# Kernel tuning notes

Hardware: AMD Instinct MI355X
Metric: run time of the kernel (lower is better)

## Reference

```python
import jax, jax.numpy as jnp
import numpy as np
import math

NUM_HEADS = 16
NUM_BUCKETS = 32
MAX_DISTANCE = 128
ALPHA = 32.0


def _rel_bucket(rel_pos):
    # bidirectional T5-style bucketing
    nb = NUM_BUCKETS // 2
    buckets = (rel_pos > 0).astype(jnp.int32) * nb
    rel_pos = jnp.abs(rel_pos)
    max_exact = nb // 2
    is_small = rel_pos < max_exact
    large = max_exact + (
        jnp.log(rel_pos.astype(jnp.float32) / max_exact + 1e-06)
        / math.log(MAX_DISTANCE / max_exact)
        * (nb - max_exact)
    ).astype(jnp.int32)
    large = jnp.minimum(large, nb - 1)
    return buckets + jnp.where(is_small, rel_pos, large)


def setup_inputs() -> dict:
    key = jax.random.key(0)
    ks = jax.random.split(key, 12)
    T, B, E = 1024, 4, 1024
    hd = E // NUM_HEADS
    s = 0.02
    f32 = jnp.float32
    return {
        "query": jax.random.normal(ks[0], (T, B, E), f32),
        "q_w": jax.random.normal(ks[1], (E, E), f32) * s,
        "q_b": jnp.zeros((E,), f32),
        "k_w": jax.random.normal(ks[2], (E, E), f32) * s,
        "k_b": jnp.zeros((E,), f32),
        "v_w": jax.random.normal(ks[3], (E, E), f32) * s,
        "v_b": jnp.zeros((E,), f32),
        "out_w": jax.random.normal(ks[4], (E, E), f32) * s,
        "out_b": jnp.zeros((E,), f32),
        "rel_emb": jax.random.normal(ks[5], (NUM_BUCKETS, NUM_HEADS), f32) * 0.1,
        "grep_w": jax.random.normal(ks[6], (hd, 8), f32) * s,
        "grep_b": jnp.zeros((8,), f32),
        "grep_a": jnp.ones((1, NUM_HEADS, 1, 1), f32),
        "bias_k": jax.random.normal(ks[7], (1, 1, E), f32) * s,
        "bias_v": jax.random.normal(ks[8], (1, 1, E), f32) * s,
    }


def reference(query, q_w, q_b, k_w, k_b, v_w, v_b, out_w, out_b,
              rel_emb, grep_w, grep_b, grep_a, bias_k, bias_v):
    tgt_len, bsz, embed_dim = query.shape
    nh = NUM_HEADS
    hd = embed_dim // nh
    scaling = hd ** (-0.5)

    # projections (self-attention: q, k, v all from query)
    q = query @ q_w + q_b
    k = query @ k_w + k_b
    v = query @ v_w + v_b
    q = q * scaling / ALPHA

    # bias_kv concat along sequence axis
    k = jnp.concatenate([k, jnp.tile(bias_k, (1, bsz, 1))], axis=0)
    v = jnp.concatenate([v, jnp.tile(bias_v, (1, bsz, 1))], axis=0)

    # faithful to source layout (including its (bsz,tgt,nh,hd)->(bsz*nh,tgt,hd) reshape)
    q = jnp.transpose(q.reshape(tgt_len, bsz, nh, hd), (1, 0, 2, 3)).reshape(bsz * nh, tgt_len, hd)
    k = jnp.transpose(k.reshape(-1, bsz, nh, hd), (1, 0, 2, 3)).reshape(bsz * nh, -1, hd)
    v = jnp.transpose(v.reshape(-1, bsz, nh, hd), (1, 0, 2, 3)).reshape(bsz * nh, -1, hd)
    src_len = k.shape[1]

    # [B*H, T, S]
    attn_weights = jnp.einsum("bth,bsh->bts", q, k)

    # T5-style relative position bias
    rel_pos = jnp.arange(src_len)[None, :] - jnp.arange(tgt_len)[:, None]
    buckets = _rel_bucket(rel_pos)                        # [T, S]
    pb = rel_emb[buckets]                                 # [T, S, H]
    pb = jnp.transpose(pb, (2, 0, 1))                     # [H, T, S]
    pb = jnp.tile(pb[None], (bsz, 1, 1, 1)).reshape(bsz * nh, tgt_len, src_len)

    # GRU-style gating of the position bias
    query_layer = q.reshape(bsz, nh, tgt_len, hd) * ALPHA / scaling
    gate = jax.nn.sigmoid((query_layer @ grep_w + grep_b).sum(-1, keepdims=True))
    gate = (gate * grep_a).reshape(bsz * nh, tgt_len, 1)
    attn_weights = attn_weights + gate * pb

    probs = jax.nn.softmax(attn_weights, axis=-1)
    attn = jnp.einsum("bts,bsh->bth", probs, v)           # [B*H, T, hd]
    attn = attn.reshape(bsz, nh, tgt_len, hd)
    attn = jnp.transpose(attn, (2, 0, 1, 3)).reshape(tgt_len, bsz, embed_dim)
    return attn @ out_w + out_b
```

## Files before the change

### kernel.cpp

```cpp
#include <hip/hip_runtime.h>
#include <stdint.h>

typedef unsigned short u16;
typedef __attribute__((ext_vector_type(4))) float  f32x4;
typedef __attribute__((ext_vector_type(8))) short  short8;
typedef __attribute__((ext_vector_type(8))) u16    u16x8;
typedef __attribute__((ext_vector_type(4))) u16    u16x4;
typedef __attribute__((ext_vector_type(4))) float  fv4;

#define T_LEN 1024
#define EMB   1024
#define SPAD  1088
#define LOG2E 1.44269504f

#define OFF_QX   (0ull)
#define OFF_VT   (0ull)
#define OFF_WT   (8912896ull)
#define OFF_QB   (17301504ull)
#define OFF_KB   (25690112ull)
#define OFF_VB   (34603008ull)
#define OFF_AT   (34603008ull)
#define OFF_GATE (43515904ull)
#define OFF_PB   (43778048ull)
#define OFF_AUX  (43909120ull)

__device__ __forceinline__ u16 f2bf(float f) {
  uint32_t u = __builtin_bit_cast(uint32_t, f);
  u += 0x7FFFu + ((u >> 16) & 1u);
  return (u16)(u >> 16);
}
__device__ __forceinline__ float bf2f(u16 s) {
  uint32_t u = ((uint32_t)s) << 16;
  return __builtin_bit_cast(float, u);
}
__device__ __forceinline__ void gld_lds16(const void* gp, void* lp) {
  __builtin_amdgcn_global_load_lds(
      (const __attribute__((address_space(1))) uint32_t*)(uintptr_t)(gp),
      (__attribute__((address_space(3))) uint32_t*)(uintptr_t)(lp),
      16, 0, 0);
}

__global__ void k_convert_q(const float* __restrict__ q, u16* __restrict__ qx) {
  int i = blockIdx.x * 256 + threadIdx.x;
  fv4 v = *((const fv4*)q + i);
  u16x4 o = { f2bf(v[0]), f2bf(v[1]), f2bf(v[2]), f2bf(v[3]) };
  *((u16x4*)qx + i) = o;
}

__global__ void k_transw(const float* __restrict__ w0, const float* __restrict__ w1,
                         const float* __restrict__ w2, const float* __restrict__ w3,
                         u16* __restrict__ wt) {
  __shared__ float tile[32][33];
  const int z = blockIdx.z;
  const float* w = (z == 0) ? w0 : (z == 1) ? w1 : (z == 2) ? w2 : w3;
  const int r0 = blockIdx.y * 32, c0 = blockIdx.x * 32;
  const int tx = threadIdx.x, ty = threadIdx.y;
  #pragma unroll
  for (int j = 0; j < 32; j += 8)
    tile[ty + j][tx] = w[(size_t)(r0 + ty + j) * EMB + c0 + tx];
  __syncthreads();
  u16* o = wt + (size_t)z * EMB * EMB;
  #pragma unroll
  for (int j = 0; j < 32; j += 8)
    o[(size_t)(c0 + ty + j) * EMB + r0 + tx] = f2bf(tile[tx][ty + j]);
}

__global__ void k_pb(const float* __restrict__ rel_emb, float* __restrict__ pbtab,
                     const float* __restrict__ grep_w, const float* __restrict__ grep_b,
                     float* __restrict__ aux) {
  int i = blockIdx.x * 256 + threadIdx.x;
  int rel = 1024 - i;
  int bucket = (rel > 0) ? 16 : 0;
  int r = rel < 0 ? -rel : rel;
  int bidx;
  if (r < 8) bidx = r;
  else {
    float lf = __logf((float)r / 8.0f + 1e-6f) * (1.0f / logf(16.0f)) * 8.0f;
    int large = 8 + (int)lf;
    bidx = large < 15 ? large : 15;
  }
  bucket += bidx;
  #pragma unroll
  for (int h = 0; h < 16; ++h) pbtab[h * 2048 + i] = rel_emb[bucket * 16 + h] * LOG2E;
  if (blockIdx.x == 0) {
    if (threadIdx.x < 64) {
      float s = 0.f;
      #pragma unroll
      for (int j = 0; j < 8; ++j) s += grep_w[threadIdx.x * 8 + j];
      aux[threadIdx.x] = s;
    } else if (threadIdx.x == 64) {
      float s = 0.f;
      #pragma unroll
      for (int j = 0; j < 8; ++j) s += grep_b[j];
      aux[64] = s;
    }
  }
}

__device__ __forceinline__ void gemm_tile(const u16* __restrict__ A, const u16* __restrict__ Bt,
                                          int m0, int n0, u16* As, u16* Bs, f32x4 acc[4][4]) {
  const int tid = threadIdx.x;
  const int lane = tid & 63, wid = tid >> 6;
  const int wm = wid >> 1, wn = wid & 1;
  const int l15 = lane & 15, l4 = lane >> 4;
  for (int kt = 0; kt < EMB; kt += 32) {
    #pragma unroll
    for (int i = 0; i < 2; ++i) {
      int cw = wid * 64 + i * 256;
      int c = cw + lane;
      int row = c >> 2, cb = c & 3;
      gld_lds16(A  + (size_t)(m0 + row) * EMB + kt + cb * 8, (char*)As + (size_t)cw * 16);
      gld_lds16(Bt + (size_t)(n0 + row) * EMB + kt + cb * 8, (char*)Bs + (size_t)cw * 16);
    }
    __syncthreads();
    short8 a[4], b[4];
    #pragma unroll
    for (int f = 0; f < 4; ++f) {
      a[f] = *(const short8*)(As + (wm * 64 + f * 16 + l15) * 32 + l4 * 8);
      b[f] = *(const short8*)(Bs + (wn * 64 + f * 16 + l15) * 32 + l4 * 8);
    }
    #pragma unroll
    for (int mi = 0; mi < 4; ++mi)
      #pragma unroll
      for (int ni = 0; ni < 4; ++ni)
        acc[mi][ni] = __builtin_amdgcn_mfma_f32_16x16x32_bf16(a[mi], b[ni], acc[mi][ni], 0, 0, 0);
    __syncthreads();
  }
}

__global__ __launch_bounds__(256, 2) void k_qkv_gemm(const u16* __restrict__ qx, const u16* __restrict__ wt,
    const float* __restrict__ qbias, const float* __restrict__ kbias, const float* __restrict__ vbias,
    u16* __restrict__ qb, u16* __restrict__ kb, u16* __restrict__ vb) {
  __shared__ u16 lds[8192];
  f32x4 acc[4][4];
  #pragma unroll
  for (int i = 0; i < 4; ++i)
    #pragma unroll
    for (int j = 0; j < 4; ++j) acc[i][j] = (f32x4){0.f, 0.f, 0.f, 0.f};
  const int m0 = blockIdx.y * 128, n0g = blockIdx.x * 128;
  gemm_tile(qx, wt, m0, n0g, lds, lds + 4096, acc);
  const int z = n0g >> 10;
  const float* bias = (z == 0) ? qbias : (z == 1) ? kbias : vbias;
  const int lane = threadIdx.x & 63, wid = threadIdx.x >> 6;
  const int wm = wid >> 1, wn = wid & 1, l15 = lane & 15, l4 = lane >> 4;
  #pragma unroll
  for (int ni = 0; ni < 4; ++ni) {
    int colg = n0g + wn * 64 + ni * 16 + l15;
    int col = colg & 1023;
    float bv = bias[col];
    int h = col >> 6, d = col & 63;
    #pragma unroll
    for (int mi = 0; mi < 4; ++mi) {
      #pragma unroll
      for (int r = 0; r < 4; ++r) {
        int row = m0 + wm * 64 + mi * 16 + l4 * 4 + r;
        int t = row >> 2, b = row & 3;
        float v = acc[mi][ni][r] + bv;
        if (z == 0) {
          int x = b * 16 + (t >> 6), u = ((t & 63) << 4) + h;
          qb[((size_t)x * 1024 + u) * 64 + d] = f2bf(v * (LOG2E / 256.0f));
        } else {
          int w = t * 16 + h;
          int j = w / 1025;
          int u = w - j * 1025;
          int x = b * 16 + j;
          if (z == 1) kb[((size_t)x * SPAD + u) * 64 + d] = f2bf(v);
          else        vb[((size_t)x * SPAD + u) * 64 + d] = f2bf(v);
        }
      }
    }
  }
}

__global__ void k_biaskv(const float* __restrict__ bias_k, const float* __restrict__ bias_v,
                         u16* __restrict__ kb, u16* __restrict__ vb) {
  int i = blockIdx.x * 256 + threadIdx.x;
  int b = i >> 10, h = (i >> 6) & 15, d = i & 63;
  int x = b * 16 + 15, u = 1009 + h;
  kb[((size_t)x * SPAD + u) * 64 + d] = f2bf(bias_k[h * 64 + d]);
  vb[((size_t)x * SPAD + u) * 64 + d] = f2bf(bias_v[h * 64 + d]);
}

__global__ void k_vtrans(const u16* __restrict__ vb, u16* __restrict__ vt) {
  __shared__ u16 t[64][72];
  const int x = blockIdx.y;
  const int u0 = blockIdx.x * 64;
  const int tid = threadIdx.x;
  const int ur = tid >> 2, c0 = (tid & 3) * 16;
  const u16* src = vb + ((size_t)x * SPAD + u0 + ur) * 64 + c0;
  u16x8 a0 = *(const u16x8*)(src);
  u16x8 a1 = *(const u16x8*)(src + 8);
  *(u16x8*)(&t[ur][c0]) = a0;
  *(u16x8*)(&t[ur][c0 + 8]) = a1;
  __syncthreads();
  const int d = tid >> 2, j = tid & 3;
  u16x8 o0, o1;
  #pragma unroll
  for (int i = 0; i < 8; ++i) o0[i] = t[j * 16 + i][d];
  #pragma unroll
  for (int i = 0; i < 8; ++i) o1[i] = t[j * 16 + 8 + i][d];
  u16* dst = vt + ((size_t)x * 64 + d) * SPAD + u0 + j * 16;
  *(u16x8*)(dst) = o0;
  *(u16x8*)(dst + 8) = o1;
}

__global__ void k_gate(const u16* __restrict__ qb, const float* __restrict__ aux,
                       const float* __restrict__ grep_a, float* __restrict__ gate) {
  int tid = threadIdx.x, lane = tid & 63, wid = tid >> 6;
  int row0 = (blockIdx.x * 4 + wid) * 8;
  int sub = lane >> 3, d0 = (lane & 7) * 8;
  int item = row0 + sub;
  u16x8 q8 = *(const u16x8*)(qb + (size_t)item * 64 + d0);
  float acc = 0.f;
  #pragma unroll
  for (int j = 0; j < 8; ++j) acc += bf2f(q8[j]) * aux[d0 + j];
  acc += __shfl_xor(acc, 1);
  acc += __shfl_xor(acc, 2);
  acc += __shfl_xor(acc, 4);
  if ((lane & 7) == 0) {
    float v = acc * (256.0f / LOG2E) + aux[64];
    float s = 1.0f / (1.0f + __expf(-v));
    gate[item] = s * grep_a[(item >> 10) & 15];
  }
}

__global__ __launch_bounds__(256, 2) void k_attn(const u16* __restrict__ qb, const u16* __restrict__ kb,
    const u16* __restrict__ vt, const float* __restrict__ gate, const float* __restrict__ pbt,
    u16* __restrict__ at) {
  __shared__ float pb_s[2048];
  __shared__ u16 Ksh[2 * 4096];
  __shared__ u16 Vsh[2 * 4096];
  __shared__ u16 Psh[4 * 2048];
  const int tid = threadIdx.x, lane = tid & 63, wid = tid >> 6;
  const int l15 = lane & 15, l4 = lane >> 4;
  const int bid = blockIdx.x;
  const int x = (bid & 7) + ((bid >> 6) << 3);
  const int tblk = (bid >> 3) & 7;
  const int h = x & 15, b = x >> 4;
  const int qrow0 = tblk * 128 + wid * 32;

  #pragma unroll
  for (int i = 0; i < 2; ++i) {
    int idx = (tid + i * 256) * 4;
    *(fv4*)(pb_s + idx) = *(const fv4*)(pbt + (size_t)h * 2048 + idx);
  }

  short8 qa[2][2];
  #pragma unroll
  for (int pf = 0; pf < 2; ++pf)
    #pragma unroll
    for (int ks = 0; ks < 2; ++ks)
      qa[pf][ks] = *(const short8*)(qb + ((size_t)x * 1024 + qrow0 + pf * 16 + l15) * 64 + ks * 32 + l4 * 8);
  float g[2][4];
  #pragma unroll
  for (int pf = 0; pf < 2; ++pf)
    #pragma unroll
    for (int r = 0; r < 4; ++r)
      g[pf][r] = gate[(size_t)x * 1024 + qrow0 + pf * 16 + l4 * 4 + r];

  const u16* kbx = kb + (size_t)x * SPAD * 64;
  const u16* vtx = vt + (size_t)x * 64 * SPAD;
  const int ra = tid >> 3, sa = tid & 7;
  const int rb = ra + 32;
  const u16* sK0 = kbx + ra * 64 + ((sa * 8) ^ ((ra & 7) << 3));
  const u16* sK1 = kbx + rb * 64 + ((sa * 8) ^ ((rb & 7) << 3));
  const u16* sV0 = vtx + (size_t)ra * SPAD + ((sa * 8) ^ ((ra & 7) << 3));
  const u16* sV1 = vtx + (size_t)rb * SPAD + ((sa * 8) ^ ((rb & 7) << 3));

  const int swz = (l15 & 7) << 3;
  int kfO[4][2];
  #pragma unroll
  for (int f = 0; f < 4; ++f)
    #pragma unroll
    for (int ks = 0; ks < 2; ++ks)
      kfO[f][ks] = (f * 16 + l15) * 64 + ((ks * 32 + l4 * 8) ^ swz);
  int paO[2][2];
  #pragma unroll
  for (int pf = 0; pf < 2; ++pf)
    #pragma unroll
    for (int ks = 0; ks < 2; ++ks)
      paO[pf][ks] = (pf * 16 + l15) * 64 + ((ks * 32 + l4 * 8) ^ swz);
  u16* Pw = Psh + wid * 2048;

  f32x4 O[2][4];
  float l_[2][4];
  #pragma unroll
  for (int pf = 0; pf < 2; ++pf) {
    #pragma unroll
    for (int df = 0; df < 4; ++df) O[pf][df] = (f32x4){0.f, 0.f, 0.f, 0.f};
    #pragma unroll
    for (int r = 0; r < 4; ++r) l_[pf][r] = 0.f;
  }

  gld_lds16(sK0, (char*)Ksh + wid * 1024);
  gld_lds16(sK1, (char*)Ksh + 4096 + wid * 1024);
  gld_lds16(sV0, (char*)Vsh + wid * 1024);
  gld_lds16(sV1, (char*)Vsh + 4096 + wid * 1024);
  sK0 += 4096; sK1 += 4096; sV0 += 64; sV1 += 64;
  __asm__ volatile("s_waitcnt vmcnt(0)" ::: "memory");
  __syncthreads();

  int cur = 0;
  for (int ic = 0; ic < 16; ++ic) {
    const int nxt = cur ^ 1;
    char* Kn = (char*)(Ksh + nxt * 4096);
    char* Vn = (char*)(Vsh + nxt * 4096);
    if (ic < 15) {
      gld_lds16(sK0, Kn + wid * 1024);
      gld_lds16(sK1, Kn + 4096 + wid * 1024);
      gld_lds16(sV0, Vn + wid * 1024);
      gld_lds16(sV1, Vn + 4096 + wid * 1024);
      sK0 += 4096; sK1 += 4096; sV0 += 64; sV1 += 64;
    } else if (wid < 2) {
      int ro = (wid * 64 + lane) >> 3, so = lane & 7;
      gld_lds16(kbx + (size_t)(1024 + ro) * 64 + so * 8, Kn + wid * 1024);
    }
    const u16* Kc = Ksh + cur * 4096;
    const u16* Vc = Vsh + cur * 4096;

    f32x4 sc[2][4];
    #pragma unroll
    for (int pf = 0; pf < 2; ++pf)
      #pragma unroll
      for (int nf = 0; nf < 4; ++nf) sc[pf][nf] = (f32x4){0.f, 0.f, 0.f, 0.f};
    #pragma unroll
    for (int nf = 0; nf < 4; ++nf)
      #pragma unroll
      for (int ks = 0; ks < 2; ++ks) {
        short8 kf = *(const short8*)(Kc + kfO[nf][ks]);
        sc[0][nf] = __builtin_amdgcn_mfma_f32_16x16x32_bf16(qa[0][ks], kf, sc[0][nf], 0, 0, 0);
        sc[1][nf] = __builtin_amdgcn_mfma_f32_16x16x32_bf16(qa[1][ks], kf, sc[1][nf], 0, 0, 0);
      }

    #pragma unroll
    for (int pf = 0; pf < 2; ++pf)
      #pragma unroll
      for (int nf = 0; nf < 4; ++nf) {
        const int base = 1024 + qrow0 + pf * 16 + l4 * 4 - (ic * 64 + nf * 16 + l15);
        #pragma unroll
        for (int r = 0; r < 4; ++r) {
          float sv = sc[pf][nf][r] + g[pf][r] * pb_s[base + r];
          float p = exp2f(sv);
          l_[pf][r] += p;
          const int prow = pf * 16 + l4 * 4 + r;
          Pw[prow * 64 + ((nf * 16 + l15) ^ ((prow & 7) << 3))] =
              (u16)(__builtin_bit_cast(uint32_t, p) >> 16);
        }
      }
    __asm__ volatile("s_waitcnt lgkmcnt(0)" ::: "memory");
    __builtin_amdgcn_sched_barrier(0);

    #pragma unroll
    for (int ks = 0; ks < 2; ++ks) {
      short8 pa0 = *(const short8*)(Pw + paO[0][ks]);
      short8 pa1 = *(const short8*)(Pw + paO[1][ks]);
      #pragma unroll
      for (int df = 0; df < 4; ++df) {
        short8 vbf = *(const short8*)(Vc + kfO[df][ks]);
        O[0][df] = __builtin_amdgcn_mfma_f32_16x16x32_bf16(pa0, vbf, O[0][df], 0, 0, 0);
        O[1][df] = __builtin_amdgcn_mfma_f32_16x16x32_bf16(pa1, vbf, O[1][df], 0, 0, 0);
      }
    }
    __asm__ volatile("s_waitcnt vmcnt(0)" ::: "memory");
    __syncthreads();
    cur = nxt;
  }

  const u16* Kt = Ksh + cur * 4096;
  short8 kt0 = *(const short8*)(Kt + l15 * 64 + l4 * 8);
  short8 kt1 = *(const short8*)(Kt + l15 * 64 + 32 + l4 * 8);
  f32x4 sc0[2];
  #pragma unroll
  for (int pf = 0; pf < 2; ++pf) {
    sc0[pf] = (f32x4){0.f, 0.f, 0.f, 0.f};
    sc0[pf] = __builtin_amdgcn_mfma_f32_16x16x32_bf16(qa[pf][0], kt0, sc0[pf], 0, 0, 0);
    sc0[pf] = __builtin_amdgcn_mfma_f32_16x16x32_bf16(qa[pf][1], kt1, sc0[pf], 0, 0, 0);
  }
  float vtail[4];
  #pragma unroll
  for (int df = 0; df < 4; ++df)
    vtail[df] = bf2f(vt[((size_t)x * 64 + df * 16 + l15) * SPAD + 1024]);

  float pt[2][4], linv[2][4];
  #pragma unroll
  for (int pf = 0; pf < 2; ++pf)
    #pragma unroll
    for (int r = 0; r < 4; ++r) {
      float dotv = __shfl(sc0[pf][r], lane & 48);
      int t = qrow0 + pf * 16 + l4 * 4 + r;
      float se = dotv + g[pf][r] * pb_s[t];
      float p = exp2f(se);
      float ls = l_[pf][r];
      ls += __shfl_xor(ls, 1);
      ls += __shfl_xor(ls, 2);
      ls += __shfl_xor(ls, 4);
      ls += __shfl_xor(ls, 8);
      pt[pf][r] = p;
      linv[pf][r] = 1.0f / (ls + p);
    }

  #pragma unroll
  for (int pf = 0; pf < 2; ++pf)
    #pragma unroll
    for (int df = 0; df < 4; ++df)
      #pragma unroll
      for (int r = 0; r < 4; ++r) {
        int t = qrow0 + pf * 16 + l4 * 4 + r;
        float o = (O[pf][df][r] + pt[pf][r] * vtail[df]) * linv[pf][r];
        at[((size_t)(t * 4 + b)) * 1024 + h * 64 + df * 16 + l15] = f2bf(o);
      }
}

__global__ __launch_bounds__(256, 2) void k_out_gemm(const u16* __restrict__ at, const u16* __restrict__ wt3,
                                                     const float* __restrict__ obias, float* __restrict__ out) {
  __shared__ u16 lds[8192];
  f32x4 acc[4][4];
  #pragma unroll
  for (int i = 0; i < 4; ++i)
    #pragma unroll
    for (int j = 0; j < 4; ++j) acc[i][j] = (f32x4){0.f, 0.f, 0.f, 0.f};
  const int m0 = blockIdx.y * 128, n0 = blockIdx.x * 128;
  gemm_tile(at, wt3, m0, n0, lds, lds + 4096, acc);
  const int lane = threadIdx.x & 63, wid = threadIdx.x >> 6;
  const int wm = wid >> 1, wn = wid & 1, l15 = lane & 15, l4 = lane >> 4;
  #pragma unroll
  for (int ni = 0; ni < 4; ++ni) {
    int col = n0 + wn * 64 + ni * 16 + l15;
    float bv = obias[col];
    #pragma unroll
    for (int mi = 0; mi < 4; ++mi) {
      #pragma unroll
      for (int r = 0; r < 4; ++r) {
        int row = m0 + wm * 64 + mi * 16 + l4 * 4 + r;
        out[(size_t)row * 1024 + col] = acc[mi][ni][r] + bv;
      }
    }
  }
}

extern "C" void kernel_launch(void* const* d_in, const int* in_sizes, int n_in,
                              void* d_out, int out_size, void* d_ws, size_t ws_size,
                              hipStream_t stream) {
  const float* query   = (const float*)d_in[0];
  const float* q_w     = (const float*)d_in[1];
  const float* q_b     = (const float*)d_in[2];
  const float* k_w     = (const float*)d_in[3];
  const float* k_b     = (const float*)d_in[4];
  const float* v_w     = (const float*)d_in[5];
  const float* v_b     = (const float*)d_in[6];
  const float* out_w   = (const float*)d_in[7];
  const float* out_b   = (const float*)d_in[8];
  const float* rel_emb = (const float*)d_in[9];
  const float* grep_w  = (const float*)d_in[10];
  const float* grep_b  = (const float*)d_in[11];
  const float* grep_a  = (const float*)d_in[12];
  const float* bias_k  = (const float*)d_in[13];
  const float* bias_v  = (const float*)d_in[14];
  char* ws = (char*)d_ws;
  u16*   qx  = (u16*)(ws + OFF_QX);
  u16*   vt  = (u16*)(ws + OFF_VT);
  u16*   wt  = (u16*)(ws + OFF_WT);
  u16*   qb  = (u16*)(ws + OFF_QB);
  u16*   kb  = (u16*)(ws + OFF_KB);
  u16*   vb  = (u16*)(ws + OFF_VB);
  u16*   at  = (u16*)(ws + OFF_AT);
  float* gate = (float*)(ws + OFF_GATE);
  float* pbt  = (float*)(ws + OFF_PB);
  float* aux  = (float*)(ws + OFF_AUX);
  float* out  = (float*)d_out;

  k_convert_q<<<dim3(4096), dim3(256), 0, stream>>>(query, qx);
  k_transw<<<dim3(32, 32, 4), dim3(32, 8), 0, stream>>>(q_w, k_w, v_w, out_w, wt);
  k_pb<<<dim3(8), dim3(256), 0, stream>>>(rel_emb, pbt, grep_w, grep_b, aux);
  k_qkv_gemm<<<dim3(24, 32), dim3(256), 0, stream>>>(qx, wt, q_b, k_b, v_b, qb, kb, vb);
  k_biaskv<<<dim3(16), dim3(256), 0, stream>>>(bias_k, bias_v, kb, vb);
  k_vtrans<<<dim3(17, 64), dim3(256), 0, stream>>>(vb, vt);
  k_gate<<<dim3(2048), dim3(256), 0, stream>>>(qb, aux, grep_a, gate);
  k_attn<<<dim3(512), dim3(256), 0, stream>>>(qb, kb, vt, gate, pbt, at);
  k_out_gemm<<<dim3(8, 32), dim3(256), 0, stream>>>(at, wt + (size_t)3 * EMB * EMB, out_b, out);
}
```

Before: 218.5 us.

## Restructure attention kernel to 32x32 MFMA with register-resident P and direct K/V loads

Rewrites the attention kernel to use 32x32x16 bf16 MFMA with transposed operand roles, so the score tile lands in registers in the layout needed for the PV product. Probabilities are packed to bf16 pairs and exchanged across half-waves with shuffles instead of going through LDS. The LDS double-buffering of K/V and the per-iteration barriers are dropped; each wave loads K/V fragments directly from global memory. This removes LDS traffic and synchronisation, but every wave now re-fetches the same K/V tiles from global/L2 and no loads are prefetched ahead.

```diff
diff --git a/kernel.cpp b/kernel.cpp
--- a/kernel.cpp
+++ b/kernel.cpp
@@ -2,11 +2,14 @@
 #include <stdint.h>
 
 typedef unsigned short u16;
-typedef __attribute__((ext_vector_type(4))) float  f32x4;
-typedef __attribute__((ext_vector_type(8))) short  short8;
-typedef __attribute__((ext_vector_type(8))) u16    u16x8;
-typedef __attribute__((ext_vector_type(4))) u16    u16x4;
-typedef __attribute__((ext_vector_type(4))) float  fv4;
+typedef unsigned int   u32;
+typedef __attribute__((ext_vector_type(4)))  float f32x4;
+typedef __attribute__((ext_vector_type(16))) float f32x16;
+typedef __attribute__((ext_vector_type(8)))  short short8;
+typedef __attribute__((ext_vector_type(8)))  u16   u16x8;
+typedef __attribute__((ext_vector_type(4)))  u16   u16x4;
+typedef __attribute__((ext_vector_type(4)))  u32   u32x4;
+typedef __attribute__((ext_vector_type(4)))  float fv4;
 
 #define T_LEN 1024
 #define EMB   1024
@@ -228,16 +231,13 @@
     const u16* __restrict__ vt, const float* __restrict__ gate, const float* __restrict__ pbt,
     u16* __restrict__ at) {
   __shared__ float pb_s[2048];
-  __shared__ u16 Ksh[2 * 4096];
-  __shared__ u16 Vsh[2 * 4096];
-  __shared__ u16 Psh[4 * 2048];
   const int tid = threadIdx.x, lane = tid & 63, wid = tid >> 6;
-  const int l15 = lane & 15, l4 = lane >> 4;
+  const int l31 = lane & 31, l5 = lane >> 5;
   const int bid = blockIdx.x;
   const int x = (bid & 7) + ((bid >> 6) << 3);
   const int tblk = (bid >> 3) & 7;
   const int h = x & 15, b = x >> 4;
-  const int qrow0 = tblk * 128 + wid * 32;
+  const int T = tblk * 128 + wid * 32 + l31;
 
   #pragma unroll
   for (int i = 0; i < 2; ++i) {
@@ -245,170 +245,114 @@
     *(fv4*)(pb_s + idx) = *(const fv4*)(pbt + (size_t)h * 2048 + idx);
   }
 
-  short8 qa[2][2];
-  #pragma unroll
-  for (int pf = 0; pf < 2; ++pf)
-    #pragma unroll
-    for (int ks = 0; ks < 2; ++ks)
-      qa[pf][ks] = *(const short8*)(qb + ((size_t)x * 1024 + qrow0 + pf * 16 + l15) * 64 + ks * 32 + l4 * 8);
-  float g[2][4];
-  #pragma unroll
-  for (int pf = 0; pf < 2; ++pf)
-    #pragma unroll
-    for (int r = 0; r < 4; ++r)
-      g[pf][r] = gate[(size_t)x * 1024 + qrow0 + pf * 16 + l4 * 4 + r];
+  short8 qf[4];
+  #pragma unroll
+  for (int c = 0; c < 4; ++c)
+    qf[c] = *(const short8*)(qb + ((size_t)x * 1024 + T) * 64 + c * 16 + l5 * 8);
+  const float g = gate[(size_t)x * 1024 + T];
 
   const u16* kbx = kb + (size_t)x * SPAD * 64;
   const u16* vtx = vt + (size_t)x * 64 * SPAD;
-  const int ra = tid >> 3, sa = tid & 7;
-  const int rb = ra + 32;
-  const u16* sK0 = kbx + ra * 64 + ((sa * 8) ^ ((ra & 7) << 3));
-  const u16* sK1 = kbx + rb * 64 + ((sa * 8) ^ ((rb & 7) << 3));
-  const u16* sV0 = vtx + (size_t)ra * SPAD + ((sa * 8) ^ ((ra & 7) << 3));
-  const u16* sV1 = vtx + (size_t)rb * SPAD + ((sa * 8) ^ ((rb & 7) << 3));
-
-  const int swz = (l15 & 7) << 3;
-  int kfO[4][2];
-  #pragma unroll
-  for (int f = 0; f < 4; ++f)
-    #pragma unroll
-    for (int ks = 0; ks < 2; ++ks)
-      kfO[f][ks] = (f * 16 + l15) * 64 + ((ks * 32 + l4 * 8) ^ swz);
-  int paO[2][2];
-  #pragma unroll
-  for (int pf = 0; pf < 2; ++pf)
-    #pragma unroll
-    for (int ks = 0; ks < 2; ++ks)
-      paO[pf][ks] = (pf * 16 + l15) * 64 + ((ks * 32 + l4 * 8) ^ swz);
-  u16* Pw = Psh + wid * 2048;
-
-  f32x4 O[2][4];
-  float l_[2][4];
-  #pragma unroll
-  for (int pf = 0; pf < 2; ++pf) {
-    #pragma unroll
-    for (int df = 0; df < 4; ++df) O[pf][df] = (f32x4){0.f, 0.f, 0.f, 0.f};
-    #pragma unroll
-    for (int r = 0; r < 4; ++r) l_[pf][r] = 0.f;
-  }
-
-  gld_lds16(sK0, (char*)Ksh + wid * 1024);
-  gld_lds16(sK1, (char*)Ksh + 4096 + wid * 1024);
-  gld_lds16(sV0, (char*)Vsh + wid * 1024);
-  gld_lds16(sV1, (char*)Vsh + 4096 + wid * 1024);
-  sK0 += 4096; sK1 += 4096; sV0 += 64; sV1 += 64;
-  __asm__ volatile("s_waitcnt vmcnt(0)" ::: "memory");
+
+  f32x16 O0 = {}, O1 = {};
+  float lsum = 0.f;
   __syncthreads();
 
-  int cur = 0;
   for (int ic = 0; ic < 16; ++ic) {
-    const int nxt = cur ^ 1;
-    char* Kn = (char*)(Ksh + nxt * 4096);
-    char* Vn = (char*)(Vsh + nxt * 4096);
-    if (ic < 15) {
-      gld_lds16(sK0, Kn + wid * 1024);
-      gld_lds16(sK1, Kn + 4096 + wid * 1024);
-      gld_lds16(sV0, Vn + wid * 1024);
-      gld_lds16(sV1, Vn + 4096 + wid * 1024);
-      sK0 += 4096; sK1 += 4096; sV0 += 64; sV1 += 64;
-    } else if (wid < 2) {
-      int ro = (wid * 64 + lane) >> 3, so = lane & 7;
-      gld_lds16(kbx + (size_t)(1024 + ro) * 64 + so * 8, Kn + wid * 1024);
-    }
-    const u16* Kc = Ksh + cur * 4096;
-    const u16* Vc = Vsh + cur * 4096;
-
-    f32x4 sc[2][4];
-    #pragma unroll
-    for (int pf = 0; pf < 2; ++pf)
-      #pragma unroll
-      for (int nf = 0; nf < 4; ++nf) sc[pf][nf] = (f32x4){0.f, 0.f, 0.f, 0.f};
-    #pragma unroll
-    for (int nf = 0; nf < 4; ++nf)
-      #pragma unroll
-      for (int ks = 0; ks < 2; ++ks) {
-        short8 kf = *(const short8*)(Kc + kfO[nf][ks]);
-        sc[0][nf] = __builtin_amdgcn_mfma_f32_16x16x32_bf16(qa[0][ks], kf, sc[0][nf], 0, 0, 0);
-        sc[1][nf] = __builtin_amdgcn_mfma_f32_16x16x32_bf16(qa[1][ks], kf, sc[1][nf], 0, 0, 0);
+    const int s0 = ic * 64;
+    short8 ka[2][4];
+    #pragma unroll
+    for (int ss = 0; ss < 2; ++ss)
+      #pragma unroll
+      for (int c = 0; c < 4; ++c)
+        ka[ss][c] = *(const short8*)(kbx + (size_t)(s0 + ss * 32 + l31) * 64 + c * 16 + l5 * 8);
+    f32x16 sc0 = {}, sc1 = {};
+    #pragma unroll
+    for (int c = 0; c < 4; ++c) {
+      sc0 = __builtin_amdgcn_mfma_f32_32x32x16_bf16(ka[0][c], qf[c], sc0, 0, 0, 0);
+      sc1 = __builtin_amdgcn_mfma_f32_32x32x16_bf16(ka[1][c], qf[c], sc1, 0, 0, 0);
+    }
+    short8 va[2][4];
+    #pragma unroll
+    for (int ds = 0; ds < 2; ++ds)
+      #pragma unroll
+      for (int c = 0; c < 4; ++c)
+        va[ds][c] = *(const short8*)(vtx + (size_t)(ds * 32 + l31) * SPAD + s0 + c * 16 + l5 * 8);
+
+    const int base = 1024 + T - s0;
+    u32 pk[16];
+    #pragma unroll
+    for (int r = 0; r < 16; r += 2) {
+      int soff = (r & 3) + 8 * (r >> 2) + 4 * l5;
+      float p0 = exp2f(sc0[r]     + g * pb_s[base - soff]);
+      float p1 = exp2f(sc0[r + 1] + g * pb_s[base - soff - 1]);
+      lsum += p0 + p1;
+      pk[r >> 1] = (__builtin_bit_cast(u32, p1) & 0xFFFF0000u) |
+                   (__builtin_bit_cast(u32, p0) >> 16);
+    }
+    #pragma unroll
+    for (int r = 0; r < 16; r += 2) {
+      int soff = 32 + (r & 3) + 8 * (r >> 2) + 4 * l5;
+      float p0 = exp2f(sc1[r]     + g * pb_s[base - soff]);
+      float p1 = exp2f(sc1[r + 1] + g * pb_s[base - soff - 1]);
+      lsum += p0 + p1;
+      pk[8 + (r >> 1)] = (__builtin_bit_cast(u32, p1) & 0xFFFF0000u) |
+                         (__builtin_bit_cast(u32, p0) >> 16);
+    }
+
+    const bool lo = (l5 == 0);
+    #pragma unroll
+    for (int ss = 0; ss < 2; ++ss) {
+      u32 X0 = (u32)__shfl_xor((int)pk[ss * 8 + 0], 32);
+      u32 X1 = (u32)__shfl_xor((int)pk[ss * 8 + 1], 32);
+      u32 X2 = (u32)__shfl_xor((int)pk[ss * 8 + 2], 32);
+      u32 X3 = (u32)__shfl_xor((int)pk[ss * 8 + 3], 32);
+      u32x4 f0 = { lo ? pk[ss * 8 + 0] : X2, lo ? pk[ss * 8 + 1] : X3,
+                   lo ? X0 : pk[ss * 8 + 2], lo ? X1 : pk[ss * 8 + 3] };
+      short8 pf0 = __builtin_bit_cast(short8, f0);
+      O0 = __builtin_amdgcn_mfma_f32_32x32x16_bf16(va[0][ss * 2], pf0, O0, 0, 0, 0);
+      O1 = __builtin_amdgcn_mfma_f32_32x32x16_bf16(va[1][ss * 2], pf0, O1, 0, 0, 0);
+      u32 Y0 = (u32)__shfl_xor((int)pk[ss * 8 + 4], 32);
+      u32 Y1 = (u32)__shfl_xor((int)pk[ss * 8 + 5], 32);
+      u32 Y2 = (u32)__shfl_xor((int)pk[ss * 8 + 6], 32);
+      u32 Y3 = (u32)__shfl_xor((int)pk[ss * 8 + 7], 32);
+      u32x4 f1 = { lo ? pk[ss * 8 + 4] : Y2, lo ? pk[ss * 8 + 5] : Y3,
+                   lo ? Y0 : pk[ss * 8 + 6], lo ? Y1 : pk[ss * 8 + 7] };
+      short8 pf1 = __builtin_bit_cast(short8, f1);
+      O0 = __builtin_amdgcn_mfma_f32_32x32x16_bf16(va[0][ss * 2 + 1], pf1, O0, 0, 0, 0);
+      O1 = __builtin_amdgcn_mfma_f32_32x32x16_bf16(va[1][ss * 2 + 1], pf1, O1, 0, 0, 0);
+    }
+  }
+
+  float dot = 0.f;
+  #pragma unroll
+  for (int c = 0; c < 4; ++c) {
+    short8 kt = *(const short8*)(kbx + (size_t)1024 * 64 + c * 16 + l5 * 8);
+    #pragma unroll
+    for (int j = 0; j < 8; ++j)
+      dot += bf2f((u16)qf[c][j]) * bf2f((u16)kt[j]);
+  }
+  dot += __shfl_xor(dot, 32);
+  float se = dot + g * pb_s[T];
+  float p_t = exp2f(se);
+  lsum += __shfl_xor(lsum, 32);
+  float linv = 1.0f / (lsum + p_t);
+
+  #pragma unroll
+  for (int ds = 0; ds < 2; ++ds) {
+    #pragma unroll
+    for (int q2 = 0; q2 < 4; ++q2) {
+      int d0 = ds * 32 + q2 * 8 + l5 * 4;
+      u16x4 ov;
+      #pragma unroll
+      for (int e = 0; e < 4; ++e) {
+        float vtl = bf2f(vtx[(size_t)(d0 + e) * SPAD + 1024]);
+        float o = ((ds ? O1[q2 * 4 + e] : O0[q2 * 4 + e]) + p_t * vtl) * linv;
+        ov[e] = f2bf(o);
       }
-
-    #pragma unroll
-    for (int pf = 0; pf < 2; ++pf)
-      #pragma unroll
-      for (int nf = 0; nf < 4; ++nf) {
-        const int base = 1024 + qrow0 + pf * 16 + l4 * 4 - (ic * 64 + nf * 16 + l15);
-        #pragma unroll
-        for (int r = 0; r < 4; ++r) {
-          float sv = sc[pf][nf][r] + g[pf][r] * pb_s[base + r];
-          float p = exp2f(sv);
-          l_[pf][r] += p;
-          const int prow = pf * 16 + l4 * 4 + r;
-          Pw[prow * 64 + ((nf * 16 + l15) ^ ((prow & 7) << 3))] =
-              (u16)(__builtin_bit_cast(uint32_t, p) >> 16);
-        }
-      }
-    __asm__ volatile("s_waitcnt lgkmcnt(0)" ::: "memory");
-    __builtin_amdgcn_sched_barrier(0);
-
-    #pragma unroll
-    for (int ks = 0; ks < 2; ++ks) {
-      short8 pa0 = *(const short8*)(Pw + paO[0][ks]);
-      short8 pa1 = *(const short8*)(Pw + paO[1][ks]);
-      #pragma unroll
-      for (int df = 0; df < 4; ++df) {
-        short8 vbf = *(const short8*)(Vc + kfO[df][ks]);
-        O[0][df] = __builtin_amdgcn_mfma_f32_16x16x32_bf16(pa0, vbf, O[0][df], 0, 0, 0);
-        O[1][df] = __builtin_amdgcn_mfma_f32_16x16x32_bf16(pa1, vbf, O[1][df], 0, 0, 0);
-      }
-    }
-    __asm__ volatile("s_waitcnt vmcnt(0)" ::: "memory");
-    __syncthreads();
-    cur = nxt;
-  }
-
-  const u16* Kt = Ksh + cur * 4096;
-  short8 kt0 = *(const short8*)(Kt + l15 * 64 + l4 * 8);
-  short8 kt1 = *(const short8*)(Kt + l15 * 64 + 32 + l4 * 8);
-  f32x4 sc0[2];
-  #pragma unroll
-  for (int pf = 0; pf < 2; ++pf) {
-    sc0[pf] = (f32x4){0.f, 0.f, 0.f, 0.f};
-    sc0[pf] = __builtin_amdgcn_mfma_f32_16x16x32_bf16(qa[pf][0], kt0, sc0[pf], 0, 0, 0);
-    sc0[pf] = __builtin_amdgcn_mfma_f32_16x16x32_bf16(qa[pf][1], kt1, sc0[pf], 0, 0, 0);
-  }
-  float vtail[4];
-  #pragma unroll
-  for (int df = 0; df < 4; ++df)
-    vtail[df] = bf2f(vt[((size_t)x * 64 + df * 16 + l15) * SPAD + 1024]);
-
-  float pt[2][4], linv[2][4];
-  #pragma unroll
-  for (int pf = 0; pf < 2; ++pf)
-    #pragma unroll
-    for (int r = 0; r < 4; ++r) {
-      float dotv = __shfl(sc0[pf][r], lane & 48);
-      int t = qrow0 + pf * 16 + l4 * 4 + r;
-      float se = dotv + g[pf][r] * pb_s[t];
-      float p = exp2f(se);
-      float ls = l_[pf][r];
-      ls += __shfl_xor(ls, 1);
-      ls += __shfl_xor(ls, 2);
-      ls += __shfl_xor(ls, 4);
-      ls += __shfl_xor(ls, 8);
-      pt[pf][r] = p;
-      linv[pf][r] = 1.0f / (ls + p);
-    }
-
-  #pragma unroll
-  for (int pf = 0; pf < 2; ++pf)
-    #pragma unroll
-    for (int df = 0; df < 4; ++df)
-      #pragma unroll
-      for (int r = 0; r < 4; ++r) {
-        int t = qrow0 + pf * 16 + l4 * 4 + r;
-        float o = (O[pf][df][r] + pt[pf][r] * vtail[df]) * linv[pf][r];
-        at[((size_t)(t * 4 + b)) * 1024 + h * 64 + df * 16 + l15] = f2bf(o);
-      }
+      *(u16x4*)(at + ((size_t)(T * 4 + b)) * 1024 + h * 64 + d0) = ov;
+    }
+  }
 }
 
 __global__ __launch_bounds__(256, 2) void k_out_gemm(const u16* __restrict__ at, const u16* __restrict__ wt3,
```

After: 248.9 us. +13.9%, slower.

## Merge prep and mid-stage kernels; use constant position bias for far tiles

Applied to the files above, without the earlier changes.

Folds the bf16 conversion, weight transposes and position-bias table build into one launch. Folds the bias_kv write, V transpose and gate computation into a second launch, cutting seven small launches down to two. In the attention kernel, tiles whose relative distance is always in the saturated bucket read a single constant bias value instead of per-element LDS lookups. The added branching raises code size and register pressure in the hot loop. The saturation thresholds must exactly match the bucketing, which depends on this specific sequence length and bucket layout.

```diff
diff --git a/kernel.cpp b/kernel.cpp
--- a/kernel.cpp
+++ b/kernel.cpp
@@ -2,11 +2,12 @@
 #include <stdint.h>
 
 typedef unsigned short u16;
-typedef __attribute__((ext_vector_type(4))) float  f32x4;
-typedef __attribute__((ext_vector_type(8))) short  short8;
-typedef __attribute__((ext_vector_type(8))) u16    u16x8;
-typedef __attribute__((ext_vector_type(4))) u16    u16x4;
-typedef __attribute__((ext_vector_type(4))) float  fv4;
+typedef unsigned int   u32;
+typedef __attribute__((ext_vector_type(4)))  float f32x4;
+typedef __attribute__((ext_vector_type(8)))  short short8;
+typedef __attribute__((ext_vector_type(8)))  u16   u16x8;
+typedef __attribute__((ext_vector_type(4)))  u16   u16x4;
+typedef __attribute__((ext_vector_type(4)))  float fv4;
 
 #define T_LEN 1024
 #define EMB   1024
@@ -40,59 +41,61 @@
       16, 0, 0);
 }
 
-__global__ void k_convert_q(const float* __restrict__ q, u16* __restrict__ qx) {
-  int i = blockIdx.x * 256 + threadIdx.x;
-  fv4 v = *((const fv4*)q + i);
-  u16x4 o = { f2bf(v[0]), f2bf(v[1]), f2bf(v[2]), f2bf(v[3]) };
-  *((u16x4*)qx + i) = o;
-}
-
-__global__ void k_transw(const float* __restrict__ w0, const float* __restrict__ w1,
-                         const float* __restrict__ w2, const float* __restrict__ w3,
-                         u16* __restrict__ wt) {
+__global__ void k_prep(const float* __restrict__ q, u16* __restrict__ qx,
+                       const float* __restrict__ w0, const float* __restrict__ w1,
+                       const float* __restrict__ w2, const float* __restrict__ w3,
+                       u16* __restrict__ wt,
+                       const float* __restrict__ rel_emb, float* __restrict__ pbtab,
+                       const float* __restrict__ grep_w, const float* __restrict__ grep_b,
+                       float* __restrict__ aux) {
   __shared__ float tile[32][33];
-  const int z = blockIdx.z;
-  const float* w = (z == 0) ? w0 : (z == 1) ? w1 : (z == 2) ? w2 : w3;
-  const int r0 = blockIdx.y * 32, c0 = blockIdx.x * 32;
-  const int tx = threadIdx.x, ty = threadIdx.y;
-  #pragma unroll
-  for (int j = 0; j < 32; j += 8)
-    tile[ty + j][tx] = w[(size_t)(r0 + ty + j) * EMB + c0 + tx];
-  __syncthreads();
-  u16* o = wt + (size_t)z * EMB * EMB;
-  #pragma unroll
-  for (int j = 0; j < 32; j += 8)
-    o[(size_t)(c0 + ty + j) * EMB + r0 + tx] = f2bf(tile[tx][ty + j]);
-}
-
-__global__ void k_pb(const float* __restrict__ rel_emb, float* __restrict__ pbtab,
-                     const float* __restrict__ grep_w, const float* __restrict__ grep_b,
-                     float* __restrict__ aux) {
-  int i = blockIdx.x * 256 + threadIdx.x;
-  int rel = 1024 - i;
-  int bucket = (rel > 0) ? 16 : 0;
-  int r = rel < 0 ? -rel : rel;
-  int bidx;
-  if (r < 8) bidx = r;
-  else {
-    float lf = __logf((float)r / 8.0f + 1e-6f) * (1.0f / logf(16.0f)) * 8.0f;
-    int large = 8 + (int)lf;
-    bidx = large < 15 ? large : 15;
-  }
-  bucket += bidx;
-  #pragma unroll
-  for (int h = 0; h < 16; ++h) pbtab[h * 2048 + i] = rel_emb[bucket * 16 + h] * LOG2E;
-  if (blockIdx.x == 0) {
-    if (threadIdx.x < 64) {
-      float s = 0.f;
-      #pragma unroll
-      for (int j = 0; j < 8; ++j) s += grep_w[threadIdx.x * 8 + j];
-      aux[threadIdx.x] = s;
-    } else if (threadIdx.x == 64) {
-      float s = 0.f;
-      #pragma unroll
-      for (int j = 0; j < 8; ++j) s += grep_b[j];
-      aux[64] = s;
+  const int bid = blockIdx.x, tid = threadIdx.x;
+  if (bid < 4096) {
+    int i = bid * 256 + tid;
+    fv4 v = *((const fv4*)q + i);
+    u16x4 o = { f2bf(v[0]), f2bf(v[1]), f2bf(v[2]), f2bf(v[3]) };
+    *((u16x4*)qx + i) = o;
+  } else if (bid < 8192) {
+    int b2 = bid - 4096;
+    int z = b2 >> 10, xy = b2 & 1023;
+    int r0 = (xy >> 5) * 32, c0 = (xy & 31) * 32;
+    const float* w = (z == 0) ? w0 : (z == 1) ? w1 : (z == 2) ? w2 : w3;
+    int tx = tid & 31, ty = tid >> 5;
+    #pragma unroll
+    for (int j = 0; j < 32; j += 8)
+      tile[ty + j][tx] = w[(size_t)(r0 + ty + j) * EMB + c0 + tx];
+    __syncthreads();
+    u16* o = wt + (size_t)z * EMB * EMB;
+    #pragma unroll
+    for (int j = 0; j < 32; j += 8)
+      o[(size_t)(c0 + ty + j) * EMB + r0 + tx] = f2bf(tile[tx][ty + j]);
+  } else {
+    int i = (bid - 8192) * 256 + tid;
+    int rel = 1024 - i;
+    int bucket = (rel > 0) ? 16 : 0;
+    int r = rel < 0 ? -rel : rel;
+    int bidx;
+    if (r < 8) bidx = r;
+    else {
+      float lf = __logf((float)r / 8.0f + 1e-6f) * (1.0f / logf(16.0f)) * 8.0f;
+      int large = 8 + (int)lf;
+      bidx = large < 15 ? large : 15;
+    }
+    bucket += bidx;
+    #pragma unroll
+    for (int hh = 0; hh < 16; ++hh) pbtab[hh * 2048 + i] = rel_emb[bucket * 16 + hh] * LOG2E;
+    if (bid == 8192) {
+      if (tid < 64) {
+        float s = 0.f;
+        #pragma unroll
+        for (int j = 0; j < 8; ++j) s += grep_w[tid * 8 + j];
+        aux[tid] = s;
+      } else if (tid == 64) {
+        float s = 0.f;
+        #pragma unroll
+        for (int j = 0; j < 8; ++j) s += grep_b[j];
+        aux[64] = s;
+      }
     }
   }
 }
@@ -172,55 +175,63 @@
   }
 }
 
-__global__ void k_biaskv(const float* __restrict__ bias_k, const float* __restrict__ bias_v,
-                         u16* __restrict__ kb, u16* __restrict__ vb) {
-  int i = blockIdx.x * 256 + threadIdx.x;
-  int b = i >> 10, h = (i >> 6) & 15, d = i & 63;
-  int x = b * 16 + 15, u = 1009 + h;
-  kb[((size_t)x * SPAD + u) * 64 + d] = f2bf(bias_k[h * 64 + d]);
-  vb[((size_t)x * SPAD + u) * 64 + d] = f2bf(bias_v[h * 64 + d]);
-}
-
-__global__ void k_vtrans(const u16* __restrict__ vb, u16* __restrict__ vt) {
+__global__ void k_mid(const u16* __restrict__ vb, u16* __restrict__ vt, u16* __restrict__ kb,
+                      const float* __restrict__ bias_k, const float* __restrict__ bias_v,
+                      const u16* __restrict__ qb, const float* __restrict__ aux,
+                      const float* __restrict__ grep_a, float* __restrict__ gate) {
   __shared__ u16 t[64][72];
-  const int x = blockIdx.y;
-  const int u0 = blockIdx.x * 64;
-  const int tid = threadIdx.x;
-  const int ur = tid >> 2, c0 = (tid & 3) * 16;
-  const u16* src = vb + ((size_t)x * SPAD + u0 + ur) * 64 + c0;
-  u16x8 a0 = *(const u16x8*)(src);
-  u16x8 a1 = *(const u16x8*)(src + 8);
-  *(u16x8*)(&t[ur][c0]) = a0;
-  *(u16x8*)(&t[ur][c0 + 8]) = a1;
-  __syncthreads();
-  const int d = tid >> 2, j = tid & 3;
-  u16x8 o0, o1;
-  #pragma unroll
-  for (int i = 0; i < 8; ++i) o0[i] = t[j * 16 + i][d];
-  #pragma unroll
-  for (int i = 0; i < 8; ++i) o1[i] = t[j * 16 + 8 + i][d];
-  u16* dst = vt + ((size_t)x * 64 + d) * SPAD + u0 + j * 16;
-  *(u16x8*)(dst) = o0;
-  *(u16x8*)(dst + 8) = o1;
-}
-
-__global__ void k_gate(const u16* __restrict__ qb, const float* __restrict__ aux,
-                       const float* __restrict__ grep_a, float* __restrict__ gate) {
-  int tid = threadIdx.x, lane = tid & 63, wid = tid >> 6;
-  int row0 = (blockIdx.x * 4 + wid) * 8;
-  int sub = lane >> 3, d0 = (lane & 7) * 8;
-  int item = row0 + sub;
-  u16x8 q8 = *(const u16x8*)(qb + (size_t)item * 64 + d0);
-  float acc = 0.f;
-  #pragma unroll
-  for (int j = 0; j < 8; ++j) acc += bf2f(q8[j]) * aux[d0 + j];
-  acc += __shfl_xor(acc, 1);
-  acc += __shfl_xor(acc, 2);
-  acc += __shfl_xor(acc, 4);
-  if ((lane & 7) == 0) {
-    float v = acc * (256.0f / LOG2E) + aux[64];
-    float s = 1.0f / (1.0f + __expf(-v));
-    gate[item] = s * grep_a[(item >> 10) & 15];
+  const int bid = blockIdx.x, tid = threadIdx.x;
+  if (bid < 1088) {
+    const int x = bid / 17, uc = bid - (bid / 17) * 17;
+    const int u0 = uc * 64;
+    const int ur = tid >> 2, c0 = (tid & 3) * 16;
+    const u16* src = vb + ((size_t)x * SPAD + u0 + ur) * 64 + c0;
+    u16x8 a0 = *(const u16x8*)(src);
+    u16x8 a1 = *(const u16x8*)(src + 8);
+    const int ug = u0 + ur;
+    if ((x & 15) == 15 && ug >= 1009 && ug <= 1024) {
+      const float* bs = bias_v + (ug - 1009) * 64 + c0;
+      #pragma unroll
+      for (int i = 0; i < 8; ++i) { a0[i] = f2bf(bs[i]); a1[i] = f2bf(bs[8 + i]); }
+    }
+    *(u16x8*)(&t[ur][c0]) = a0;
+    *(u16x8*)(&t[ur][c0 + 8]) = a1;
+    __syncthreads();
+    const int d = tid >> 2, j = tid & 3;
+    u16x8 o0, o1;
+    #pragma unroll
+    for (int i = 0; i < 8; ++i) o0[i] = t[j * 16 + i][d];
+    #pragma unroll
+    for (int i = 0; i < 8; ++i) o1[i] = t[j * 16 + 8 + i][d];
+    u16* dst = vt + ((size_t)x * 64 + d) * SPAD + u0 + j * 16;
+    *(u16x8*)(dst) = o0;
+    *(u16x8*)(dst + 8) = o1;
+    if ((x & 15) == 15 && uc == 16) {
+      int k = tid * 4;
+      int hh = k >> 6, dd = k & 63;
+      u16x4 kv;
+      #pragma unroll
+      for (int e = 0; e < 4; ++e) kv[e] = f2bf(bias_k[hh * 64 + dd + e]);
+      *(u16x4*)(kb + ((size_t)x * SPAD + 1009 + hh) * 64 + dd) = kv;
+    }
+  } else {
+    int gb = bid - 1088;
+    int lane = tid & 63, wid = tid >> 6;
+    int row0 = (gb * 4 + wid) * 8;
+    int sub = lane >> 3, d0 = (lane & 7) * 8;
+    int item = row0 + sub;
+    u16x8 q8 = *(const u16x8*)(qb + (size_t)item * 64 + d0);
+    float acc = 0.f;
+    #pragma unroll
+    for (int j = 0; j < 8; ++j) acc += bf2f(q8[j]) * aux[d0 + j];
+    acc += __shfl_xor(acc, 1);
+    acc += __shfl_xor(acc, 2);
+    acc += __shfl_xor(acc, 4);
+    if ((lane & 7) == 0) {
+      float v = acc * (256.0f / LOG2E) + aux[64];
+      float s = 1.0f / (1.0f + __expf(-v));
+      gate[item] = s * grep_a[(item >> 10) & 15];
+    }
   }
 }
 
@@ -332,21 +343,42 @@
         sc[1][nf] = __builtin_amdgcn_mfma_f32_16x16x32_bf16(qa[1][ks], kf, sc[1][nf], 0, 0, 0);
       }
 
-    #pragma unroll
-    for (int pf = 0; pf < 2; ++pf)
-      #pragma unroll
-      for (int nf = 0; nf < 4; ++nf) {
-        const int base = 1024 + qrow0 + pf * 16 + l4 * 4 - (ic * 64 + nf * 16 + l15);
+    const int s0 = ic * 64;
+    const bool farN = (s0 <= qrow0 - 191);
+    const bool farP = (s0 >= qrow0 + 159);
+    if (farN | farP) {
+      const float pbF = farN ? pb_s[1300] : pb_s[800];
+      #pragma unroll
+      for (int pf = 0; pf < 2; ++pf)
         #pragma unroll
-        for (int r = 0; r < 4; ++r) {
-          float sv = sc[pf][nf][r] + g[pf][r] * pb_s[base + r];
-          float p = exp2f(sv);
-          l_[pf][r] += p;
-          const int prow = pf * 16 + l4 * 4 + r;
-          Pw[prow * 64 + ((nf * 16 + l15) ^ ((prow & 7) << 3))] =
-              (u16)(__builtin_bit_cast(uint32_t, p) >> 16);
+        for (int nf = 0; nf < 4; ++nf) {
+          #pragma unroll
+          for (int r = 0; r < 4; ++r) {
+            float sv = sc[pf][nf][r] + g[pf][r] * pbF;
+            float p = exp2f(sv);
+            l_[pf][r] += p;
+            const int prow = pf * 16 + l4 * 4 + r;
+            Pw[prow * 64 + ((nf * 16 + l15) ^ ((prow & 7) << 3))] =
+                (u16)(__builtin_bit_cast(uint32_t, p) >> 16);
+          }
         }
-      }
+    } else {
+      #pragma unroll
+      for (int pf = 0; pf < 2; ++pf)
+        #pragma unroll
+        for (int nf = 0; nf < 4; ++nf) {
+          const int base = 1024 + qrow0 + pf * 16 + l4 * 4 - (s0 + nf * 16 + l15);
+          #pragma unroll
+          for (int r = 0; r < 4; ++r) {
+            float sv = sc[pf][nf][r] + g[pf][r] * pb_s[base + r];
+            float p = exp2f(sv);
+            l_[pf][r] += p;
+            const int prow = pf * 16 + l4 * 4 + r;
+            Pw[prow * 64 + ((nf * 16 + l15) ^ ((prow & 7) << 3))] =
+                (u16)(__builtin_bit_cast(uint32_t, p) >> 16);
+          }
+        }
+    }
     __asm__ volatile("s_waitcnt lgkmcnt(0)" ::: "memory");
     __builtin_amdgcn_sched_barrier(0);
 
@@ -469,13 +501,10 @@
   float* aux  = (float*)(ws + OFF_AUX);
   float* out  = (float*)d_out;
 
-  k_convert_q<<<dim3(4096), dim3(256), 0, stream>>>(query, qx);
-  k_transw<<<dim3(32, 32, 4), dim3(32, 8), 0, stream>>>(q_w, k_w, v_w, out_w, wt);
-  k_pb<<<dim3(8), dim3(256), 0, stream>>>(rel_emb, pbt, grep_w, grep_b, aux);
+  k_prep<<<dim3(8200), dim3(256), 0, stream>>>(query, qx, q_w, k_w, v_w, out_w, wt,
+                                               rel_emb, pbt, grep_w, grep_b, aux);
   k_qkv_gemm<<<dim3(24, 32), dim3(256), 0, stream>>>(qx, wt, q_b, k_b, v_b, qb, kb, vb);
-  k_biaskv<<<dim3(16), dim3(256), 0, stream>>>(bias_k, bias_v, kb, vb);
-  k_vtrans<<<dim3(17, 64), dim3(256), 0, stream>>>(vb, vt);
-  k_gate<<<dim3(2048), dim3(256), 0, stream>>>(qb, aux, grep_a, gate);
+  k_mid<<<dim3(3136), dim3(256), 0, stream>>>(vb, vt, kb, bias_k, bias_v, qb, aux, grep_a, gate);
   k_attn<<<dim3(512), dim3(256), 0, stream>>>(qb, kb, vt, gate, pbt, at);
   k_out_gemm<<<dim3(8, 32), dim3(256), 0, stream>>>(at, wt + (size_t)3 * EMB * EMB, out_b, out);
 }
```

New measurement: 210.6 us. -3.6%, faster.
